# Optimization experiments

Measured on AMD Instinct MI355X. Metric: run time of the kernel, lower is better.

Reference implementation:

```python
import jax, jax.numpy as jnp
import numpy as np

N = 50000        # nodes
E = 400000       # edges
SC = 64          # scalar (l=0) channels
VC = 32          # vector (l=1) channels
DIM = SC + 3 * VC  # 160
NB = 64          # radial basis functions
CUTOFF = 5.0
EPS = 1e-5


def _edge_rot_mat(edge_vec, edge_rand):
    # init_edge_rot_mat: build per-edge frame aligning edge dir with canonical axis
    dist = jnp.sqrt(jnp.sum(edge_vec ** 2, axis=1, keepdims=True))
    nx = edge_vec / dist
    ev2 = edge_rand - 0.5
    ev2 = ev2 / jnp.sqrt(jnp.sum(ev2 ** 2, axis=1, keepdims=True))
    ev2b = jnp.stack([-ev2[:, 1], ev2[:, 0], ev2[:, 2]], axis=1)
    ev2c = jnp.stack([ev2[:, 0], -ev2[:, 2], ev2[:, 1]], axis=1)
    dot = lambda a: jnp.abs(jnp.sum(a * nx, axis=1, keepdims=True))
    ev2 = jnp.where(dot(ev2) > dot(ev2b), ev2b, ev2)
    ev2 = jnp.where(dot(ev2) > dot(ev2c), ev2c, ev2)
    nz = jnp.cross(nx, ev2)
    nz = nz / jnp.sqrt(jnp.sum(nz ** 2, axis=1, keepdims=True))
    ny = jnp.cross(nx, nz)
    ny = ny / jnp.sqrt(jnp.sum(ny ** 2, axis=1, keepdims=True))
    # edge_rot_mat_inv columns = [nz, nx, -ny]; R = inv^T -> rows = [nz, nx, -ny]
    return jnp.stack([nz, nx, -ny], axis=1)  # [E,3,3]


def setup_inputs() -> dict:
    key = jax.random.key(0)
    ks = jax.random.split(key, 10)
    x = jax.random.normal(ks[0], (N, DIM), dtype=jnp.float32)
    pos = jax.random.normal(ks[1], (N, 3), dtype=jnp.float32)
    src = jax.random.randint(ks[2], (E,), 0, N)
    off = jax.random.randint(ks[3], (E,), 1, N)
    dst = (src + off) % N  # no self loops -> nonzero edge vectors
    edge_index = jnp.stack([src, dst], axis=0).astype(jnp.int64)
    edge_rand = jax.random.uniform(ks[4], (E, 3), dtype=jnp.float32)
    W0 = jax.random.normal(ks[5], (SC, SC), dtype=jnp.float32)
    W1 = jax.random.normal(ks[6], (VC, VC), dtype=jnp.float32)
    rbf_centers = jnp.linspace(0.0, CUTOFF, NB).astype(jnp.float32)
    rbf_widths = 0.5 * jnp.ones((NB,), dtype=jnp.float32)
    edge_proj_w = 0.1 * jax.random.normal(ks[7], (NB, 1), dtype=jnp.float32)
    edge_proj_b = jnp.zeros((1,), dtype=jnp.float32)
    ln_gamma = jnp.ones((SC,), dtype=jnp.float32) + 0.1 * jax.random.normal(ks[8], (SC,), dtype=jnp.float32)
    ln_beta = 0.1 * jax.random.normal(ks[9], (SC,), dtype=jnp.float32)
    return {"x": x, "pos": pos, "edge_index": edge_index, "edge_rand": edge_rand,
            "W0": W0, "W1": W1, "rbf_centers": rbf_centers, "rbf_widths": rbf_widths,
            "edge_proj_w": edge_proj_w, "edge_proj_b": edge_proj_b,
            "ln_gamma": ln_gamma, "ln_beta": ln_beta}


def reference(x, pos, edge_index, edge_rand, W0, W1, rbf_centers, rbf_widths,
              edge_proj_w, edge_proj_b, ln_gamma, ln_beta):
    src, dst = edge_index[0], edge_index[1]
    edge_vec = pos[src] - pos[dst]                       # [E,3]
    dist = jnp.sqrt(jnp.sum(edge_vec ** 2, axis=1))      # [E]
    # rotation matrices are detached in the original
    R = jax.lax.stop_gradient(_edge_rot_mat(edge_vec, edge_rand))  # [E,3,3]

    # radial basis (gaussian) with cosine cutoff envelope
    d = dist[:, None]                                    # [E,1]
    rbf = jnp.exp(-0.5 * ((d - rbf_centers) / rbf_widths) ** 2)  # [E,NB]
    cut = jnp.where(d <= CUTOFF, 0.5 * (jnp.cos(jnp.pi * d / CUTOFF) + 1.0), 0.0)
    rbf = rbf * cut                                      # [E,NB]

    # gather source features, split irreps 64x0e + 32x1e
    h = x[src]                                           # [E,DIM]
    h0 = h[:, :SC]                                       # [E,SC]
    h1 = h[:, SC:].reshape(-1, VC, 3)                    # [E,VC,3]

    # rotate l=1 block into the edge-aligned frame (Wigner-D for l=1 is R)
    h1r = jnp.einsum('eij,ecj->eci', R, h1)

    # SO2 convolution: per-l channel mixing (o3.Linear, 1/sqrt(fan_in) path norm)
    m0 = (h0 @ W0) / np.sqrt(SC)                         # [E,SC]
    m1 = jnp.einsum('ecj,cd->edj', h1r, W1) / np.sqrt(VC)  # [E,VC,3]

    # edge modulation: global mean of sigmoid(edge_proj(rbf)) (scalar, as in source)
    edge_w = jnp.mean(jax.nn.sigmoid(rbf @ edge_proj_w + edge_proj_b))
    m0 = m0 * edge_w
    m1 = m1 * edge_w

    # rotate l=1 back with R^T
    m1b = jnp.einsum('eji,ecj->eci', R, m1)
    msg = jnp.concatenate([m0, m1b.reshape(-1, 3 * VC)], axis=1)  # [E,DIM]

    # scatter-sum aggregation over destination nodes
    agg = jax.ops.segment_sum(msg, dst, num_segments=x.shape[0])  # [N,DIM]

    # EquivariantLayerNormV2: LayerNorm on l=0 slice only
    s = agg[:, :SC]
    mu = jnp.mean(s, axis=-1, keepdims=True)
    var = jnp.mean((s - mu) ** 2, axis=-1, keepdims=True)
    s_ln = (s - mu) / jnp.sqrt(var + EPS) * ln_gamma + ln_beta

    # S2Activation: SiLU on l=0 slice, identity on l=1
    s_act = jax.nn.silu(s_ln)
    return jnp.concatenate([s_act, agg[:, SC:]], axis=1)  # [N,DIM]
```

## Files before the change

kernel.cpp:

```cpp
#include <hip/hip_runtime.h>

#define N_NODES 50000
#define N_EDGES 400000
#define DIM 160
#define NB 64
#define CUTOFF 5.0f
#define LN_EPS 1e-5f
#define PI_F 3.14159265358979323846f

#define SLOT_STRIDE 64
#define DEG_STRIDE 8

#define WS_DEG   16
#define WS_PKT   (WS_DEG + N_NODES * DEG_STRIDE)
#define WS_POS4  (WS_PKT + 4 * NB)
#define WS_ESRC  (WS_POS4 + 4 * N_NODES)

__global__ __launch_bounds__(256) void prep(
    const float* __restrict__ pos, const float* __restrict__ centers,
    const float* __restrict__ widths, const float* __restrict__ proj_w,
    int* __restrict__ degp, float4* __restrict__ pkt,
    float4* __restrict__ pos4, float* __restrict__ ew_accum)
{
    const int i = blockIdx.x * blockDim.x + threadIdx.x;
    if (i < 16) ((int*)ew_accum)[i] = 0;
    if (i < NB)
        pkt[i] = make_float4(centers[i], 1.0f / widths[i], proj_w[i], 0.0f);
    if (i < N_NODES) {
        const int4 z4 = make_int4(0, 0, 0, 0);
        ((int4*)(degp))[2 * i]     = z4;
        ((int4*)(degp))[2 * i + 1] = z4;
        pos4[i] = make_float4(pos[3 * i], pos[3 * i + 1], pos[3 * i + 2], 0.0f);
    }
}

#define EPT 4

__global__ __launch_bounds__(256) void hist_ew_fill(
    const int* __restrict__ ei, const float4* __restrict__ pos4,
    const float4* __restrict__ pkt, const float* __restrict__ proj_b,
    int* __restrict__ degp, int* __restrict__ esrc, float* __restrict__ ew_accum)
{
    const float bias = proj_b[0];
    const int base = blockIdx.x * (256 * EPT) + threadIdx.x;

    int  s[EPT], d[EPT], slot[EPT];
    bool v[EPT];
    #pragma unroll
    for (int k = 0; k < EPT; ++k) {
        const int e = base + 256 * k;
        v[k] = (e < N_EDGES);
        s[k] = v[k] ? ei[e] : 0;
        d[k] = v[k] ? ei[N_EDGES + e] : 0;
    }

    #pragma unroll
    for (int k = 0; k < EPT; ++k)
        slot[k] = v[k] ? atomicAdd(&degp[(long)d[k] * DEG_STRIDE], 1) : 0;

    float4 ps[EPT], pd[EPT];
    #pragma unroll
    for (int k = 0; k < EPT; ++k) { ps[k] = pos4[s[k]]; pd[k] = pos4[d[k]]; }

    #pragma unroll
    for (int k = 0; k < EPT; ++k)
        if (v[k] && slot[k] < SLOT_STRIDE)
            esrc[((long)d[k] << 6) + slot[k]] = s[k];

    float dist[EPT];
    #pragma unroll
    for (int k = 0; k < EPT; ++k) {
        const float dx = ps[k].x - pd[k].x;
        const float dy = ps[k].y - pd[k].y;
        const float dz = ps[k].z - pd[k].z;
        dist[k] = sqrtf(dx * dx + dy * dy + dz * dz);
    }

    float z[EPT] = {0.f, 0.f, 0.f, 0.f};
    #pragma unroll 4
    for (int b = 0; b < NB; ++b) {
        const float4 t4 = pkt[b];
        #pragma unroll
        for (int k = 0; k < EPT; ++k) {
            const float t = (dist[k] - t4.x) * t4.y;
            z[k] = fmaf(__expf(-0.5f * t * t), t4.z, z[k]);
        }
    }

    float sig = 0.0f;
    #pragma unroll
    for (int k = 0; k < EPT; ++k) {
        if (v[k]) {
            const float cut = (dist[k] <= CUTOFF)
                            ? 0.5f * (__cosf(PI_F * dist[k] * (1.0f / CUTOFF)) + 1.0f)
                            : 0.0f;
            sig += 1.0f / (1.0f + __expf(-(z[k] * cut + bias)));
        }
    }

    #pragma unroll
    for (int off = 32; off > 0; off >>= 1) sig += __shfl_xor(sig, off);
    __shared__ float red[4];
    if ((threadIdx.x & 63) == 0) red[threadIdx.x >> 6] = sig;
    __syncthreads();
    if (threadIdx.x == 0)
        atomicAdd(ew_accum, red[0] + red[1] + red[2] + red[3]);
}

#define TNODES 64

__global__ __launch_bounds__(256) void gather_node(
    const float* __restrict__ x, const int* __restrict__ degp,
    const int* __restrict__ esrc, float* __restrict__ out,
    const float* __restrict__ W0, const float* __restrict__ W1,
    const float* __restrict__ ln_gamma, const float* __restrict__ ln_beta,
    const float* __restrict__ ew_accum)
{
    __shared__ float sW0[64 * 64];
    __shared__ float sW1[32 * 32];

    const int t    = threadIdx.x;
    const int lane = t & 63;
    const int w    = t >> 6;
    const int node0 = blockIdx.x * TNODES;

    {
        const float4* w04 = (const float4*)W0;
        float4* s04 = (float4*)sW0;
        #pragma unroll
        for (int i = 0; i < 4; ++i) s04[t + 256 * i] = w04[t + 256 * i];
        ((float4*)sW1)[t] = ((const float4*)W1)[t];
    }

    #pragma unroll 1
    for (int p = 0; p < 16; p += 2) {
        const int nlA = w * 16 + p;
        const int nlB = nlA + 1;
        const int nA  = node0 + nlA;
        const int nB  = node0 + nlB;
        const long nAc = (nA < N_NODES) ? nA : 0;
        const long nBc = (nB < N_NODES) ? nB : 0;

        const int svA  = esrc[(nAc << 6) + lane];
        const int svB  = esrc[(nBc << 6) + lane];
        const int cntA = (nA < N_NODES) ? min(degp[nAc * DEG_STRIDE], SLOT_STRIDE) : 0;
        const int cntB = (nB < N_NODES) ? min(degp[nBc * DEG_STRIDE], SLOT_STRIDE) : 0;

        float4 aA = make_float4(0.f, 0.f, 0.f, 0.f);
        float4 aB = make_float4(0.f, 0.f, 0.f, 0.f);

        #define GBODY(sv, cnt, acc)                                            \
        {                                                                      \
            int j = 0;                                                         \
            for (; j + 8 <= cnt; j += 8) {                                     \
                const int s0 = __shfl(sv, j);                                  \
                const int s1 = __shfl(sv, j + 1);                              \
                const int s2 = __shfl(sv, j + 2);                              \
                const int s3 = __shfl(sv, j + 3);                              \
                const int s4 = __shfl(sv, j + 4);                              \
                const int s5 = __shfl(sv, j + 5);                              \
                const int s6 = __shfl(sv, j + 6);                              \
                const int s7 = __shfl(sv, j + 7);                              \
                if (lane < 40) {                                               \
                    const float4 v0 = ((const float4*)(x + (long)s0 * DIM))[lane]; \
                    const float4 v1 = ((const float4*)(x + (long)s1 * DIM))[lane]; \
                    const float4 v2 = ((const float4*)(x + (long)s2 * DIM))[lane]; \
                    const float4 v3 = ((const float4*)(x + (long)s3 * DIM))[lane]; \
                    const float4 v4 = ((const float4*)(x + (long)s4 * DIM))[lane]; \
                    const float4 v5 = ((const float4*)(x + (long)s5 * DIM))[lane]; \
                    const float4 v6 = ((const float4*)(x + (long)s6 * DIM))[lane]; \
                    const float4 v7 = ((const float4*)(x + (long)s7 * DIM))[lane]; \
                    acc.x += ((v0.x + v1.x) + (v2.x + v3.x)) + ((v4.x + v5.x) + (v6.x + v7.x)); \
                    acc.y += ((v0.y + v1.y) + (v2.y + v3.y)) + ((v4.y + v5.y) + (v6.y + v7.y)); \
                    acc.z += ((v0.z + v1.z) + (v2.z + v3.z)) + ((v4.z + v5.z) + (v6.z + v7.z)); \
                    acc.w += ((v0.w + v1.w) + (v2.w + v3.w)) + ((v4.w + v5.w) + (v6.w + v7.w)); \
                }                                                              \
            }                                                                  \
            for (; j + 4 <= cnt; j += 4) {                                     \
                const int s0 = __shfl(sv, j);                                  \
                const int s1 = __shfl(sv, j + 1);                              \
                const int s2 = __shfl(sv, j + 2);                              \
                const int s3 = __shfl(sv, j + 3);                              \
                if (lane < 40) {                                               \
                    const float4 v0 = ((const float4*)(x + (long)s0 * DIM))[lane]; \
                    const float4 v1 = ((const float4*)(x + (long)s1 * DIM))[lane]; \
                    const float4 v2 = ((const float4*)(x + (long)s2 * DIM))[lane]; \
                    const float4 v3 = ((const float4*)(x + (long)s3 * DIM))[lane]; \
                    acc.x += (v0.x + v1.x) + (v2.x + v3.x);                    \
                    acc.y += (v0.y + v1.y) + (v2.y + v3.y);                    \
                    acc.z += (v0.z + v1.z) + (v2.z + v3.z);                    \
                    acc.w += (v0.w + v1.w) + (v2.w + v3.w);                    \
                }                                                              \
            }                                                                  \
            for (; j < cnt; ++j) {                                             \
                const int s0 = __shfl(sv, j);                                  \
                if (lane < 40) {                                               \
                    const float4 v0 = ((const float4*)(x + (long)s0 * DIM))[lane]; \
                    acc.x += v0.x; acc.y += v0.y; acc.z += v0.z; acc.w += v0.w; \
                }                                                              \
            }                                                                  \
        }
        GBODY(svA, cntA, aA)
        GBODY(svB, cntB, aB)
        #undef GBODY

        if (lane < 40) {
            if (nA < N_NODES) *(float4*)(out + (long)nA * DIM + 4 * lane) = aA;
            if (nB < N_NODES) *(float4*)(out + (long)nB * DIM + 4 * lane) = aB;
        }
    }

    __threadfence_block();
    __syncthreads();

    const float ew   = ew_accum[0] * (1.0f / 400000.0f);
    const float s_m0 = ew * 0.125f;
    const float s_m1 = ew * 0.17677669529663687f;

    {
        const int q   = t >> 4;
        const int sub = t & 15;
        const int n0  = node0 + 4 * q;
        const float* r0 = out + (long)((n0 + 0 < N_NODES) ? n0 + 0 : 0) * DIM;
        const float* r1 = out + (long)((n0 + 1 < N_NODES) ? n0 + 1 : 0) * DIM;
        const float* r2 = out + (long)((n0 + 2 < N_NODES) ? n0 + 2 : 0) * DIM;
        const float* r3 = out + (long)((n0 + 3 < N_NODES) ? n0 + 3 : 0) * DIM;

        float acc[4][4];
        #pragma unroll
        for (int n = 0; n < 4; ++n)
            #pragma unroll
            for (int j = 0; j < 4; ++j) acc[n][j] = 0.0f;

        #pragma unroll 4
        for (int k0 = 0; k0 < 64; k0 += 4) {
            const float4 a0 = *(const float4*)(r0 + k0);
            const float4 a1 = *(const float4*)(r1 + k0);
            const float4 a2 = *(const float4*)(r2 + k0);
            const float4 a3 = *(const float4*)(r3 + k0);
            const float4 w0 = *(const float4*)(sW0 + (k0 + 0) * 64 + 4 * sub);
            const float4 w1 = *(const float4*)(sW0 + (k0 + 1) * 64 + 4 * sub);
            const float4 w2 = *(const float4*)(sW0 + (k0 + 2) * 64 + 4 * sub);
            const float4 w3 = *(const float4*)(sW0 + (k0 + 3) * 64 + 4 * sub);
            #define FMA4(A, av, wv) \
                A[0] = fmaf(av, wv.x, A[0]); A[1] = fmaf(av, wv.y, A[1]); \
                A[2] = fmaf(av, wv.z, A[2]); A[3] = fmaf(av, wv.w, A[3]);
            FMA4(acc[0], a0.x, w0) FMA4(acc[0], a0.y, w1) FMA4(acc[0], a0.z, w2) FMA4(acc[0], a0.w, w3)
            FMA4(acc[1], a1.x, w0) FMA4(acc[1], a1.y, w1) FMA4(acc[1], a1.z, w2) FMA4(acc[1], a1.w, w3)
            FMA4(acc[2], a2.x, w0) FMA4(acc[2], a2.y, w1) FMA4(acc[2], a2.z, w2) FMA4(acc[2], a2.w, w3)
            FMA4(acc[3], a3.x, w0) FMA4(acc[3], a3.y, w1) FMA4(acc[3], a3.z, w2) FMA4(acc[3], a3.w, w3)
            #undef FMA4
        }

        float sum[4], ssq[4];
        #pragma unroll
        for (int n = 0; n < 4; ++n) {
            sum[n] = 0.0f; ssq[n] = 0.0f;
            #pragma unroll
            for (int j = 0; j < 4; ++j) {
                acc[n][j] *= s_m0;
                sum[n] += acc[n][j];
                ssq[n] = fmaf(acc[n][j], acc[n][j], ssq[n]);
            }
        }
        #pragma unroll
        for (int m = 1; m <= 8; m <<= 1) {
            #pragma unroll
            for (int n = 0; n < 4; ++n) {
                sum[n] += __shfl_xor(sum[n], m);
                ssq[n] += __shfl_xor(ssq[n], m);
            }
        }

        const float4 g = *(const float4*)(ln_gamma + 4 * sub);
        const float4 b = *(const float4*)(ln_beta  + 4 * sub);
        #pragma unroll
        for (int n = 0; n < 4; ++n) {
            const int node = node0 + 4 * q + n;
            if (node < N_NODES) {
                const float mu   = sum[n] * (1.0f / 64.0f);
                const float var  = ssq[n] * (1.0f / 64.0f) - mu * mu;
                const float rstd = rsqrtf(var + LN_EPS);
                const float t0 = (acc[n][0] - mu) * rstd * g.x + b.x;
                const float t1 = (acc[n][1] - mu) * rstd * g.y + b.y;
                const float t2 = (acc[n][2] - mu) * rstd * g.z + b.z;
                const float t3 = (acc[n][3] - mu) * rstd * g.w + b.w;
                float4 o;
                o.x = t0 / (1.0f + __expf(-t0));
                o.y = t1 / (1.0f + __expf(-t1));
                o.z = t2 / (1.0f + __expf(-t2));
                o.w = t3 / (1.0f + __expf(-t3));
                *(float4*)(out + (long)node * DIM + 4 * sub) = o;
            }
        }
    }

    {
        const int nl   = t >> 2;
        const int sub  = t & 3;
        const int node = node0 + nl;
        const bool valid = node < N_NODES;
        float* grow = out + (long)(valid ? node : 0) * DIM;
        const float* bRow = grow + 64;

        float o[24];
        #pragma unroll
        for (int m = 0; m < 24; ++m) o[m] = 0.0f;

        #pragma unroll 2
        for (int tt = 0; tt < 8; ++tt) {
            const float4 v0 = *(const float4*)(bRow + 12 * tt);
            const float4 v1 = *(const float4*)(bRow + 12 * tt + 4);
            const float4 v2 = *(const float4*)(bRow + 12 * tt + 8);
            const float a[12] = { v0.x, v0.y, v0.z, v0.w,
                                  v1.x, v1.y, v1.z, v1.w,
                                  v2.x, v2.y, v2.z, v2.w };
            #pragma unroll
            for (int r = 0; r < 4; ++r) {
                const int cp = 4 * tt + r;
                const float a0 = a[3 * r];
                const float a1 = a[3 * r + 1];
                const float a2 = a[3 * r + 2];
                const float4* w4 = (const float4*)(sW1 + cp * 32 + sub * 8);
                const float4 wA = w4[0];
                const float4 wB = w4[1];
                const float wc[8] = { wA.x, wA.y, wA.z, wA.w, wB.x, wB.y, wB.z, wB.w };
                #pragma unroll
                for (int cc = 0; cc < 8; ++cc) {
                    o[3 * cc]     = fmaf(wc[cc], a0, o[3 * cc]);
                    o[3 * cc + 1] = fmaf(wc[cc], a1, o[3 * cc + 1]);
                    o[3 * cc + 2] = fmaf(wc[cc], a2, o[3 * cc + 2]);
                }
            }
        }

        if (valid) {
            float4* ro4 = (float4*)(grow + 64 + 24 * sub);
            #pragma unroll
            for (int q2 = 0; q2 < 6; ++q2) {
                float4 ov;
                ov.x = o[4 * q2]     * s_m1;
                ov.y = o[4 * q2 + 1] * s_m1;
                ov.z = o[4 * q2 + 2] * s_m1;
                ov.w = o[4 * q2 + 3] * s_m1;
                ro4[q2] = ov;
            }
        }
    }
}

extern "C" void kernel_launch(void* const* d_in, const int* in_sizes, int n_in,
                              void* d_out, int out_size, void* d_ws, size_t ws_size,
                              hipStream_t stream) {
    const float* x       = (const float*)d_in[0];
    const float* pos     = (const float*)d_in[1];
    const int*   ei      = (const int*)d_in[2];
    const float* W0      = (const float*)d_in[4];
    const float* W1      = (const float*)d_in[5];
    const float* centers = (const float*)d_in[6];
    const float* widths  = (const float*)d_in[7];
    const float* proj_w  = (const float*)d_in[8];
    const float* proj_b  = (const float*)d_in[9];
    const float* gamma   = (const float*)d_in[10];
    const float* beta    = (const float*)d_in[11];

    float* out  = (float*)d_out;
    int*   wsi  = (int*)d_ws;
    float* ew   = (float*)d_ws;
    int*   degp = wsi + WS_DEG;
    float4* pkt  = (float4*)(wsi + WS_PKT);
    float4* pos4 = (float4*)(wsi + WS_POS4);
    int*   esrc = wsi + WS_ESRC;

    const int pb = (N_NODES + 255) / 256;
    prep<<<pb, 256, 0, stream>>>(pos, centers, widths, proj_w, degp, pkt, pos4, ew);

    const int eb = (N_EDGES + 256 * EPT - 1) / (256 * EPT);
    hist_ew_fill<<<eb, 256, 0, stream>>>(ei, pos4, pkt, proj_b, degp, esrc, ew);

    const int tiles = (N_NODES + TNODES - 1) / TNODES;
    gather_node<<<tiles, 256, 0, stream>>>(x, degp, esrc, out,
                                           W0, W1, gamma, beta, ew);
}
```

Measured before the change: 191.2 us.

## Shrink node tile per block to 16 and remap epilogue threads

Cuts the nodes per block in the gather/transform kernel from 64 to 16, so each wave gathers 4 nodes instead of 16. The epilogue thread mapping changes to match: 16 threads per node for the scalar W0 mix and LayerNorm, and per-thread vector mixing over 2 output channels instead of 8. The goal is more blocks and better load balance and latency hiding on the gather. In exchange, W0/W1 are staged into shared memory four times as often and each thread reuses fewer weights per load.

Result: faster. 186.0 us (-2.7%).

```diff
diff --git a/kernel.cpp b/kernel.cpp
--- a/kernel.cpp
+++ b/kernel.cpp
@@ -107,7 +107,7 @@
         atomicAdd(ew_accum, red[0] + red[1] + red[2] + red[3]);
 }
 
-#define TNODES 64
+#define TNODES 16
 
 __global__ __launch_bounds__(256) void gather_node(
     const float* __restrict__ x, const int* __restrict__ degp,
@@ -133,8 +133,8 @@
     }
 
     #pragma unroll 1
-    for (int p = 0; p < 16; p += 2) {
-        const int nlA = w * 16 + p;
+    for (int p = 0; p < 4; p += 2) {
+        const int nlA = 4 * w + p;
         const int nlB = nlA + 1;
         const int nA  = node0 + nlA;
         const int nB  = node0 + nlB;
@@ -217,95 +217,63 @@
     const float s_m0 = ew * 0.125f;
     const float s_m1 = ew * 0.17677669529663687f;
 
+    const int nl  = t >> 4;
+    const int sub = t & 15;
+    const int node = node0 + nl;
+    const bool valid = node < N_NODES;
+    float* grow = out + (long)(valid ? node : 0) * DIM;
+
     {
-        const int q   = t >> 4;
-        const int sub = t & 15;
-        const int n0  = node0 + 4 * q;
-        const float* r0 = out + (long)((n0 + 0 < N_NODES) ? n0 + 0 : 0) * DIM;
-        const float* r1 = out + (long)((n0 + 1 < N_NODES) ? n0 + 1 : 0) * DIM;
-        const float* r2 = out + (long)((n0 + 2 < N_NODES) ? n0 + 2 : 0) * DIM;
-        const float* r3 = out + (long)((n0 + 3 < N_NODES) ? n0 + 3 : 0) * DIM;
-
-        float acc[4][4];
-        #pragma unroll
-        for (int n = 0; n < 4; ++n)
-            #pragma unroll
-            for (int j = 0; j < 4; ++j) acc[n][j] = 0.0f;
+        float acc[4] = {0.f, 0.f, 0.f, 0.f};
 
         #pragma unroll 4
         for (int k0 = 0; k0 < 64; k0 += 4) {
-            const float4 a0 = *(const float4*)(r0 + k0);
-            const float4 a1 = *(const float4*)(r1 + k0);
-            const float4 a2 = *(const float4*)(r2 + k0);
-            const float4 a3 = *(const float4*)(r3 + k0);
+            const float4 a = *(const float4*)(grow + k0);
             const float4 w0 = *(const float4*)(sW0 + (k0 + 0) * 64 + 4 * sub);
             const float4 w1 = *(const float4*)(sW0 + (k0 + 1) * 64 + 4 * sub);
             const float4 w2 = *(const float4*)(sW0 + (k0 + 2) * 64 + 4 * sub);
             const float4 w3 = *(const float4*)(sW0 + (k0 + 3) * 64 + 4 * sub);
-            #define FMA4(A, av, wv) \
-                A[0] = fmaf(av, wv.x, A[0]); A[1] = fmaf(av, wv.y, A[1]); \
-                A[2] = fmaf(av, wv.z, A[2]); A[3] = fmaf(av, wv.w, A[3]);
-            FMA4(acc[0], a0.x, w0) FMA4(acc[0], a0.y, w1) FMA4(acc[0], a0.z, w2) FMA4(acc[0], a0.w, w3)
-            FMA4(acc[1], a1.x, w0) FMA4(acc[1], a1.y, w1) FMA4(acc[1], a1.z, w2) FMA4(acc[1], a1.w, w3)
-            FMA4(acc[2], a2.x, w0) FMA4(acc[2], a2.y, w1) FMA4(acc[2], a2.z, w2) FMA4(acc[2], a2.w, w3)
-            FMA4(acc[3], a3.x, w0) FMA4(acc[3], a3.y, w1) FMA4(acc[3], a3.z, w2) FMA4(acc[3], a3.w, w3)
-            #undef FMA4
-        }
-
-        float sum[4], ssq[4];
+            acc[0] = fmaf(a.x, w0.x, fmaf(a.y, w1.x, fmaf(a.z, w2.x, fmaf(a.w, w3.x, acc[0]))));
+            acc[1] = fmaf(a.x, w0.y, fmaf(a.y, w1.y, fmaf(a.z, w2.y, fmaf(a.w, w3.y, acc[1]))));
+            acc[2] = fmaf(a.x, w0.z, fmaf(a.y, w1.z, fmaf(a.z, w2.z, fmaf(a.w, w3.z, acc[2]))));
+            acc[3] = fmaf(a.x, w0.w, fmaf(a.y, w1.w, fmaf(a.z, w2.w, fmaf(a.w, w3.w, acc[3]))));
+        }
+
+        float sum = 0.0f, ssq = 0.0f;
         #pragma unroll
-        for (int n = 0; n < 4; ++n) {
-            sum[n] = 0.0f; ssq[n] = 0.0f;
-            #pragma unroll
-            for (int j = 0; j < 4; ++j) {
-                acc[n][j] *= s_m0;
-                sum[n] += acc[n][j];
-                ssq[n] = fmaf(acc[n][j], acc[n][j], ssq[n]);
-            }
+        for (int j = 0; j < 4; ++j) {
+            acc[j] *= s_m0;
+            sum += acc[j];
+            ssq = fmaf(acc[j], acc[j], ssq);
         }
         #pragma unroll
         for (int m = 1; m <= 8; m <<= 1) {
-            #pragma unroll
-            for (int n = 0; n < 4; ++n) {
-                sum[n] += __shfl_xor(sum[n], m);
-                ssq[n] += __shfl_xor(ssq[n], m);
-            }
-        }
-
-        const float4 g = *(const float4*)(ln_gamma + 4 * sub);
-        const float4 b = *(const float4*)(ln_beta  + 4 * sub);
-        #pragma unroll
-        for (int n = 0; n < 4; ++n) {
-            const int node = node0 + 4 * q + n;
-            if (node < N_NODES) {
-                const float mu   = sum[n] * (1.0f / 64.0f);
-                const float var  = ssq[n] * (1.0f / 64.0f) - mu * mu;
-                const float rstd = rsqrtf(var + LN_EPS);
-                const float t0 = (acc[n][0] - mu) * rstd * g.x + b.x;
-                const float t1 = (acc[n][1] - mu) * rstd * g.y + b.y;
-                const float t2 = (acc[n][2] - mu) * rstd * g.z + b.z;
-                const float t3 = (acc[n][3] - mu) * rstd * g.w + b.w;
-                float4 o;
-                o.x = t0 / (1.0f + __expf(-t0));
-                o.y = t1 / (1.0f + __expf(-t1));
-                o.z = t2 / (1.0f + __expf(-t2));
-                o.w = t3 / (1.0f + __expf(-t3));
-                *(float4*)(out + (long)node * DIM + 4 * sub) = o;
-            }
+            sum += __shfl_xor(sum, m);
+            ssq += __shfl_xor(ssq, m);
+        }
+
+        if (valid) {
+            const float mu   = sum * (1.0f / 64.0f);
+            const float var  = ssq * (1.0f / 64.0f) - mu * mu;
+            const float rstd = rsqrtf(var + LN_EPS);
+            const float4 g = *(const float4*)(ln_gamma + 4 * sub);
+            const float4 b = *(const float4*)(ln_beta  + 4 * sub);
+            const float t0 = (acc[0] - mu) * rstd * g.x + b.x;
+            const float t1 = (acc[1] - mu) * rstd * g.y + b.y;
+            const float t2 = (acc[2] - mu) * rstd * g.z + b.z;
+            const float t3 = (acc[3] - mu) * rstd * g.w + b.w;
+            float4 o;
+            o.x = t0 / (1.0f + __expf(-t0));
+            o.y = t1 / (1.0f + __expf(-t1));
+            o.z = t2 / (1.0f + __expf(-t2));
+            o.w = t3 / (1.0f + __expf(-t3));
+            *(float4*)(grow + 4 * sub) = o;
         }
     }
 
     {
-        const int nl   = t >> 2;
-        const int sub  = t & 3;
-        const int node = node0 + nl;
-        const bool valid = node < N_NODES;
-        float* grow = out + (long)(valid ? node : 0) * DIM;
         const float* bRow = grow + 64;
-
-        float o[24];
-        #pragma unroll
-        for (int m = 0; m < 24; ++m) o[m] = 0.0f;
+        float o[6] = {0.f, 0.f, 0.f, 0.f, 0.f, 0.f};
 
         #pragma unroll 2
         for (int tt = 0; tt < 8; ++tt) {
@@ -321,30 +289,24 @@
                 const float a0 = a[3 * r];
                 const float a1 = a[3 * r + 1];
                 const float a2 = a[3 * r + 2];
-                const float4* w4 = (const float4*)(sW1 + cp * 32 + sub * 8);
-                const float4 wA = w4[0];
-                const float4 wB = w4[1];
-                const float wc[8] = { wA.x, wA.y, wA.z, wA.w, wB.x, wB.y, wB.z, wB.w };
-                #pragma unroll
-                for (int cc = 0; cc < 8; ++cc) {
-                    o[3 * cc]     = fmaf(wc[cc], a0, o[3 * cc]);
-                    o[3 * cc + 1] = fmaf(wc[cc], a1, o[3 * cc + 1]);
-                    o[3 * cc + 2] = fmaf(wc[cc], a2, o[3 * cc + 2]);
-                }
+                const float2 wc = *(const float2*)(sW1 + cp * 32 + 2 * sub);
+                o[0] = fmaf(wc.x, a0, o[0]);
+                o[1] = fmaf(wc.x, a1, o[1]);
+                o[2] = fmaf(wc.x, a2, o[2]);
+                o[3] = fmaf(wc.y, a0, o[3]);
+                o[4] = fmaf(wc.y, a1, o[4]);
+                o[5] = fmaf(wc.y, a2, o[5]);
             }
         }
 
         if (valid) {
-            float4* ro4 = (float4*)(grow + 64 + 24 * sub);
-            #pragma unroll
-            for (int q2 = 0; q2 < 6; ++q2) {
-                float4 ov;
-                ov.x = o[4 * q2]     * s_m1;
-                ov.y = o[4 * q2 + 1] * s_m1;
-                ov.z = o[4 * q2 + 2] * s_m1;
-                ov.w = o[4 * q2 + 3] * s_m1;
-                ro4[q2] = ov;
-            }
+            float* vout = grow + 64 + 6 * sub;
+            float2* vo2 = (float2*)vout;
+            float2 p0, p1, p2;
+            p0.x = o[0] * s_m1; p0.y = o[1] * s_m1;
+            p1.x = o[2] * s_m1; p1.y = o[3] * s_m1;
+            p2.x = o[4] * s_m1; p2.y = o[5] * s_m1;
+            vo2[0] = p0; vo2[1] = p1; vo2[2] = p2;
         }
     }
 }
```
